# Performance work log

Hardware: AMD Instinct MI355X
Metric: run time of the kernel (lower is better)

Reference implementation:

```python
import jax, jax.numpy as jnp
import numpy as np

HIDDEN = 128
NI = 100000   # ingredient nodes
NT = 100000   # taste nodes
E = 800000    # part_of edges
EPS = 1e-5


def setup_inputs() -> dict:
    key = jax.random.key(0)
    ks = jax.random.split(key, 12)
    s = 1.0 / np.sqrt(HIDDEN)
    return {
        "x_ingredient": jax.random.normal(ks[0], (NI, HIDDEN), jnp.float32),
        "x_taste": jax.random.normal(ks[1], (NT, HIDDEN), jnp.float32),
        "edge_index": jax.random.randint(ks[2], (2, E), 0, 100000, jnp.int64),
        "W_ing": jax.random.normal(ks[3], (HIDDEN, HIDDEN), jnp.float32) * s,
        "b_ing": jax.random.normal(ks[4], (HIDDEN,), jnp.float32) * s,
        "W_taste": jax.random.normal(ks[5], (HIDDEN, HIDDEN), jnp.float32) * s,
        "b_taste": jax.random.normal(ks[6], (HIDDEN,), jnp.float32) * s,
        "att_src": jax.random.normal(ks[7], (HIDDEN,), jnp.float32) * s,
        "att_dst": jax.random.normal(ks[8], (HIDDEN,), jnp.float32) * s,
        "k_lin_W": jax.random.normal(ks[9], (HIDDEN, HIDDEN), jnp.float32) * s,
        "k_lin_b": jax.random.normal(ks[10], (HIDDEN,), jnp.float32) * s,
        "q": jax.random.normal(ks[11], (HIDDEN,), jnp.float32) * s,
        "gamma": jnp.ones((HIDDEN,), jnp.float32),
        "beta": jnp.zeros((HIDDEN,), jnp.float32),
    }


def reference(x_ingredient, x_taste, edge_index, W_ing, b_ing, W_taste, b_taste,
              att_src, att_dst, k_lin_W, k_lin_b, q, gamma, beta):
    # Per-node-type linear projection (HANConv, heads=1)
    h_src = x_ingredient @ W_ing.T + b_ing      # [NI, D]
    h_dst = x_taste @ W_taste.T + b_taste       # [NT, D]

    # Per-node attention logits
    a_src = h_src @ att_src                     # [NI]
    a_dst = h_dst @ att_dst                     # [NT]

    src, dst = edge_index[0], edge_index[1]
    alpha = jax.nn.leaky_relu(a_src[src] + a_dst[dst], negative_slope=0.2)  # [E]

    # Segment softmax over incoming edges of each taste node
    m = jax.ops.segment_max(alpha, dst, num_segments=NT)
    m = jnp.where(jnp.isfinite(m), m, 0.0)      # empty segments -> 0
    e = jnp.exp(alpha - m[dst])
    denom = jax.ops.segment_sum(e, dst, num_segments=NT)
    coef = e / jnp.where(denom[dst] == 0, 1.0, denom[dst])  # [E]

    # Weighted scatter-add aggregation, then per-metapath ReLU (as in HANConv)
    agg = jax.ops.segment_sum(coef[:, None] * h_src[src], dst, num_segments=NT)  # [NT, D]
    agg = jax.nn.relu(agg)

    # Semantic attention across metapaths (single metapath -> weight 1.0)
    w = jnp.tanh(agg @ k_lin_W.T + k_lin_b).mean(0) @ q     # scalar
    beta_sem = jax.nn.softmax(w[None])[0]                   # == 1.0
    out = beta_sem * agg

    # BatchNorm (training statistics) + ReLU
    mu = out.mean(0)
    var = out.var(0)
    out = (out - mu) / jnp.sqrt(var + EPS) * gamma + beta
    return jax.nn.relu(out)
```

## Files before the change

kernel.cpp:

```cpp
#include <hip/hip_runtime.h>
#include <hip/hip_bf16.h>

#define HIDDEN 128
#define NI_N 100000
#define NT_N 100000
#define NE_N 800000
#define EPS_F 1e-5f
#define ELLW 32
#define STATS_B 256
#define ACC_REP 32

#define NB_PROJ 782
#define NB_SC 512
#define SC_THREADS (NB_SC * 256)
#define SC_K 7
#define NB_ADST 3125
#define NB_ZERO 391

typedef __attribute__((ext_vector_type(8))) short bf16x8;
typedef __attribute__((ext_vector_type(4))) float f32x4;

static __device__ __forceinline__ unsigned short f2bf(float f) {
  unsigned u = __float_as_uint(f);
  u += 0x7FFFu + ((u >> 16) & 1u);
  return (unsigned short)(u >> 16);
}

static __device__ __forceinline__ bf16x8 pack8(float4 a, float4 b) {
  bf16x8 r;
  r[0] = (short)f2bf(a.x); r[1] = (short)f2bf(a.y);
  r[2] = (short)f2bf(a.z); r[3] = (short)f2bf(a.w);
  r[4] = (short)f2bf(b.x); r[5] = (short)f2bf(b.y);
  r[6] = (short)f2bf(b.z); r[7] = (short)f2bf(b.w);
  return r;
}

static __device__ __forceinline__ float bf_lo(unsigned int h) {
  return __uint_as_float(h << 16);
}
static __device__ __forceinline__ float bf_hi(unsigned int h) {
  return __uint_as_float(h & 0xffff0000u);
}


__global__ __launch_bounds__(256) void k_pre(const float* __restrict__ W,
                                             const float* __restrict__ b,
                                             const float* __restrict__ att,
                                             float* __restrict__ wbuf,
                                             int* __restrict__ cursor,
                                             float* __restrict__ accum,
                                             int* __restrict__ ticket) {
  int bid = blockIdx.x, t = threadIdx.x;
  if (bid < NB_ZERO) {
    int i = bid * 256 + t;
    if (i < NT_N) cursor[i] = 0;
    return;
  }
  __shared__ float red[128];
#pragma unroll
  for (int r = 0; r < ACC_REP; ++r) accum[r * 256 + t] = 0.f;
  if (t == 0) *ticket = 0;
  if (t < 128) {
    float s = 0.f;
#pragma unroll 8
    for (int c = 0; c < 128; ++c) s += att[c] * W[c * 128 + t];
    wbuf[t] = s;
    red[t] = att[t] * b[t];
  }
  __syncthreads();
  if (t < 64) {
    float v = red[t] + red[t + 64];
    v += __shfl_xor(v, 1);
    v += __shfl_xor(v, 2);
    v += __shfl_xor(v, 4);
    v += __shfl_xor(v, 8);
    v += __shfl_xor(v, 16);
    v += __shfl_xor(v, 32);
    if (t == 0) wbuf[128] = v;
  }
}

__global__ __launch_bounds__(256) void k_main(
    const float* __restrict__ x, const float* __restrict__ W,
    const float* __restrict__ bias, const float* __restrict__ att,
    unsigned int* __restrict__ h32, float* __restrict__ a_src,
    const int* __restrict__ esrc, const int* __restrict__ edst,
    int* __restrict__ cursor, int* __restrict__ ell,
    const float* __restrict__ xt, const float* __restrict__ wbuf,
    float* __restrict__ a_dst) {
  const int t = threadIdx.x;

  if (blockIdx.x >= NB_PROJ && blockIdx.x < NB_PROJ + NB_SC) {
    int base = (blockIdx.x - NB_PROJ) * 256 + t;
    int sv[SC_K], dv[SC_K];
    bool ok[SC_K];
#pragma unroll
    for (int k = 0; k < SC_K; ++k) {
      int e = base + k * SC_THREADS;
      ok[k] = e < NE_N;
      int ec = ok[k] ? e : (NE_N - 1);
      sv[k] = esrc[ec];
      dv[k] = edst[ec];
    }
#pragma unroll
    for (int k = 0; k < SC_K; ++k) {
      if (ok[k]) {
        int pos = atomicAdd(&cursor[dv[k]], 1);
        if (pos < ELLW) ell[dv[k] * ELLW + pos] = sv[k];
      }
    }
    return;
  }

  if (blockIdx.x >= NB_PROJ + NB_SC) {
    __shared__ float swe[128];
    if (t < 128) swe[t] = wbuf[t];
    __syncthreads();
    float be = wbuf[128];
    int lane = t & 63, wv = t >> 6;
    int sub = lane & 7, r = lane >> 3;
    int node = (blockIdx.x - NB_PROJ - NB_SC) * 32 + wv * 8 + r;
    if (node >= NT_N) return;
    const float* xp = xt + (size_t)node * 128 + sub * 4;
    float4 v0 = *(const float4*)(xp);
    float4 v1 = *(const float4*)(xp + 32);
    float4 v2 = *(const float4*)(xp + 64);
    float4 v3 = *(const float4*)(xp + 96);
    const float* wp = swe + sub * 4;
    float4 w0 = *(const float4*)(wp);
    float4 w1 = *(const float4*)(wp + 32);
    float4 w2 = *(const float4*)(wp + 64);
    float4 w3 = *(const float4*)(wp + 96);
    float s = v0.x * w0.x + v0.y * w0.y + v0.z * w0.z + v0.w * w0.w;
    s += v1.x * w1.x + v1.y * w1.y + v1.z * w1.z + v1.w * w1.w;
    s += v2.x * w2.x + v2.y * w2.y + v2.z * w2.z + v2.w * w2.w;
    s += v3.x * w3.x + v3.y * w3.y + v3.z * w3.z + v3.w * w3.w;
    s += __shfl_xor(s, 1);
    s += __shfl_xor(s, 2);
    s += __shfl_xor(s, 4);
    if (sub == 0) a_dst[node] = s + be;
    return;
  }

  const int bid = blockIdx.x;
  __shared__ float sh_a[128];
  if (t < 128) sh_a[t] = 0.f;
  __syncthreads();

  const int wave = t >> 6, lane = t & 63;
  const int colhalf = wave & 1, rowhalf = wave >> 1;
  const int row0 = bid * 128 + rowhalf * 64;
  const int lr = lane & 15;
  const int q = lane >> 4;

  bf16x8 bfrag[4][4];
  float bv[4], av[4];
#pragma unroll
  for (int nt = 0; nt < 4; ++nt) {
    int wrow = colhalf * 64 + nt * 16 + lr;
    const float* wp = W + wrow * 128 + q * 8;
#pragma unroll
    for (int kb = 0; kb < 4; ++kb) {
      float4 wa = *(const float4*)(wp + kb * 32);
      float4 wb = *(const float4*)(wp + kb * 32 + 4);
      bfrag[nt][kb] = pack8(wa, wb);
    }
    bv[nt] = bias[wrow];
    av[nt] = att[wrow];
  }

#pragma unroll
  for (int rt = 0; rt < 4; ++rt) {
    int arow = row0 + rt * 16 + lr;
    int rowc = (arow < NI_N) ? arow : (NI_N - 1);
    const float* xp = x + (size_t)rowc * 128 + q * 8;
    bf16x8 afrag[4];
#pragma unroll
    for (int kb = 0; kb < 4; ++kb) {
      float4 xa = *(const float4*)(xp + kb * 32);
      float4 xb = *(const float4*)(xp + kb * 32 + 4);
      afrag[kb] = pack8(xa, xb);
    }
    float part[4] = {0.f, 0.f, 0.f, 0.f};
    f32x4 cc[4];
#pragma unroll
    for (int nt = 0; nt < 4; ++nt) {
      f32x4 c = {0.f, 0.f, 0.f, 0.f};
#pragma unroll
      for (int kb = 0; kb < 4; ++kb)
        c = __builtin_amdgcn_mfma_f32_16x16x32_bf16(afrag[kb], bfrag[nt][kb], c,
                                                    0, 0, 0);
#pragma unroll
      for (int i = 0; i < 4; ++i) {
        float v = c[i] + bv[nt];
        part[i] += v * av[nt];
        c[i] = v;
      }
      cc[nt] = c;
    }
#pragma unroll
    for (int i = 0; i < 4; ++i) {
      int orow = row0 + rt * 16 + q * 4 + i;
      if (orow < NI_N) {
        unsigned u0 = (unsigned)f2bf(cc[0][i]) | ((unsigned)f2bf(cc[1][i]) << 16);
        unsigned u1 = (unsigned)f2bf(cc[2][i]) | ((unsigned)f2bf(cc[3][i]) << 16);
        unsigned int* hp = h32 + (size_t)orow * 64 + colhalf * 32 + lr;
        hp[0] = u0;
        hp[16] = u1;
      }
      float p = part[i];
      p += __shfl_xor(p, 1);
      p += __shfl_xor(p, 2);
      p += __shfl_xor(p, 4);
      p += __shfl_xor(p, 8);
      if (lr == 0)
        atomicAdd(&sh_a[rowhalf * 64 + rt * 16 + q * 4 + i], p);
    }
  }
  __syncthreads();
  if (t < 128) {
    int row = bid * 128 + t;
    if (row < NI_N) a_src[row] = sh_a[t];
  }
}

__global__ __launch_bounds__(256) void k_agg(const int* __restrict__ deg,
                                             const int* __restrict__ ell,
                                             const float* __restrict__ a_src,
                                             const float* __restrict__ a_dst,
                                             const unsigned int* __restrict__ h32,
                                             unsigned int* __restrict__ aggb) {
  int wv = (blockIdx.x * blockDim.x + threadIdx.x) >> 6;
  int lane = threadIdx.x & 63;
  int half = lane >> 5, l = lane & 31;
  int node = wv * 2 + half;
  if (node >= NT_N) return;
  int n = deg[node];
  n = (n > ELLW) ? ELLW : n;
  float ax = 0.f, ay = 0.f, bx = 0.f, by = 0.f;
  if (n > 0) {
    float ad = a_dst[node];
    int li = (l < n) ? l : (n - 1);
    int sr = ell[node * ELLW + li];
    float al = a_src[sr] + ad;
    al = (al > 0.f) ? al : 0.2f * al;
    float ex = (l < n) ? __expf(al) : 0.f;
    float den = 0.f;
    const int sb = half << 5;
    int n8 = (n + 7) & ~7;
    const uint2* h2 = (const uint2*)h32;
    for (int j = 0; j < n8; j += 8) {
      int s0 = __shfl(sr, sb + j + 0), s1 = __shfl(sr, sb + j + 1);
      int s2 = __shfl(sr, sb + j + 2), s3 = __shfl(sr, sb + j + 3);
      int s4 = __shfl(sr, sb + j + 4), s5 = __shfl(sr, sb + j + 5);
      int s6 = __shfl(sr, sb + j + 6), s7 = __shfl(sr, sb + j + 7);
      float e0 = __shfl(ex, sb + j + 0), e1 = __shfl(ex, sb + j + 1);
      float e2 = __shfl(ex, sb + j + 2), e3 = __shfl(ex, sb + j + 3);
      float e4 = __shfl(ex, sb + j + 4), e5 = __shfl(ex, sb + j + 5);
      float e6 = __shfl(ex, sb + j + 6), e7 = __shfl(ex, sb + j + 7);
      uint2 g0 = h2[s0 * 32 + l];
      uint2 g1 = h2[s1 * 32 + l];
      uint2 g2 = h2[s2 * 32 + l];
      uint2 g3 = h2[s3 * 32 + l];
      uint2 g4 = h2[s4 * 32 + l];
      uint2 g5 = h2[s5 * 32 + l];
      uint2 g6 = h2[s6 * 32 + l];
      uint2 g7 = h2[s7 * 32 + l];
      ax += e0 * bf_lo(g0.x) + e1 * bf_lo(g1.x) + e2 * bf_lo(g2.x) +
            e3 * bf_lo(g3.x) + e4 * bf_lo(g4.x) + e5 * bf_lo(g5.x) +
            e6 * bf_lo(g6.x) + e7 * bf_lo(g7.x);
      ay += e0 * bf_hi(g0.x) + e1 * bf_hi(g1.x) + e2 * bf_hi(g2.x) +
            e3 * bf_hi(g3.x) + e4 * bf_hi(g4.x) + e5 * bf_hi(g5.x) +
            e6 * bf_hi(g6.x) + e7 * bf_hi(g7.x);
      bx += e0 * bf_lo(g0.y) + e1 * bf_lo(g1.y) + e2 * bf_lo(g2.y) +
            e3 * bf_lo(g3.y) + e4 * bf_lo(g4.y) + e5 * bf_lo(g5.y) +
            e6 * bf_lo(g6.y) + e7 * bf_lo(g7.y);
      by += e0 * bf_hi(g0.y) + e1 * bf_hi(g1.y) + e2 * bf_hi(g2.y) +
            e3 * bf_hi(g3.y) + e4 * bf_hi(g4.y) + e5 * bf_hi(g5.y) +
            e6 * bf_hi(g6.y) + e7 * bf_hi(g7.y);
      den += ((e0 + e1) + (e2 + e3)) + ((e4 + e5) + (e6 + e7));
    }
    float inv = 1.f / den;
    ax *= inv; ay *= inv; bx *= inv; by *= inv;
  }
  ax = fmaxf(ax, 0.f);
  ay = fmaxf(ay, 0.f);
  bx = fmaxf(bx, 0.f);
  by = fmaxf(by, 0.f);
  uint2 o;
  o.x = (unsigned)f2bf(ax) | ((unsigned)f2bf(ay) << 16);
  o.y = (unsigned)f2bf(bx) | ((unsigned)f2bf(by) << 16);
  ((uint2*)aggb)[node * 32 + l] = o;
}

__global__ __launch_bounds__(256) void k_stats(const unsigned int* __restrict__ aggb,
                                               float* __restrict__ accum,
                                               const float* __restrict__ gamma,
                                               const float* __restrict__ beta,
                                               float* __restrict__ consts,
                                               int* __restrict__ ticket) {
  __shared__ float red[8][32][8];
  int t = threadIdx.x;
  int p2 = t & 31, g = t >> 5;
  float st[8] = {0.f, 0.f, 0.f, 0.f, 0.f, 0.f, 0.f, 0.f};
  for (int row = blockIdx.x * 8 + g; row < NT_N; row += STATS_B * 8) {
    uint2 v = ((const uint2*)(aggb + (size_t)row * 64))[p2];
    float l0 = bf_lo(v.x), h0 = bf_hi(v.x);
    float l1 = bf_lo(v.y), h1 = bf_hi(v.y);
    st[0] += l0; st[1] += l0 * l0; st[2] += h0; st[3] += h0 * h0;
    st[4] += l1; st[5] += l1 * l1; st[6] += h1; st[7] += h1 * h1;
  }
#pragma unroll
  for (int k = 0; k < 8; ++k) red[g][p2][k] = st[k];
  __syncthreads();
  {
    int p = t >> 2, slot = t & 3;
    int pp2 = p >> 1, u = p & 1;
    float s = 0.f;
#pragma unroll
    for (int gg = 0; gg < 8; ++gg) s += red[gg][pp2][u * 4 + slot];
    atomicAdd(&accum[(blockIdx.x & (ACC_REP - 1)) * 256 + t], s);
  }
  __threadfence();
  __shared__ int amLast;
  if (t == 0) amLast = (atomicAdd(ticket, 1) == STATS_B - 1);
  __syncthreads();
  if (!amLast) return;
  __threadfence();
  __shared__ float fin[256];
  {
    float s = 0.f;
#pragma unroll
    for (int r = 0; r < ACC_REP; ++r) s += accum[r * 256 + t];
    fin[t] = s;
  }
  __syncthreads();
  if (t < 128) {
    int c = t;
    int ch = c >> 6, rem = c & 63;
    int w = rem >> 5, rem2 = rem & 31;
    int half = rem2 >> 4, lr = rem2 & 15;
    int p = ch * 32 + w * 16 + lr;
    float sum = fin[p * 4 + half * 2];
    float sq = fin[p * 4 + half * 2 + 1];
    float mu = sum * (1.f / NT_N);
    float var = sq * (1.f / NT_N) - mu * mu;
    float sc = gamma[c] * rsqrtf(var + EPS_F);
    consts[c] = sc;
    consts[128 + c] = beta[c] - mu * sc;
  }
}

__global__ __launch_bounds__(256) void k_norm(const unsigned int* __restrict__ aggb,
                                              const float* __restrict__ consts,
                                              float* __restrict__ out) {
  __shared__ float sc[256];
  int t = threadIdx.x;
  sc[t] = consts[t];
  __syncthreads();
  int u = blockIdx.x * 256 + t;
  if (u >= NT_N * 16) return;
  uint4 v = ((const uint4*)aggb)[u];
  int wid = u >> 4, k = u & 15;
  int p0 = k * 4;
  int c0 = (p0 >> 5) * 64 + ((p0 >> 4) & 1) * 32 + (p0 & 15);
  unsigned vv[4] = {v.x, v.y, v.z, v.w};
  float o0[4], o1[4];
#pragma unroll
  for (int j = 0; j < 4; ++j) {
    int c = c0 + j;
    float lo = bf_lo(vv[j]), hi = bf_hi(vv[j]);
    o0[j] = fmaxf(lo * sc[c] + sc[128 + c], 0.f);
    o1[j] = fmaxf(hi * sc[c + 16] + sc[144 + c], 0.f);
  }
  float* op = out + (size_t)wid * 128 + c0;
  *(float4*)op = make_float4(o0[0], o0[1], o0[2], o0[3]);
  *(float4*)(op + 16) = make_float4(o1[0], o1[1], o1[2], o1[3]);
}

extern "C" void kernel_launch(void* const* d_in, const int* in_sizes, int n_in,
                              void* d_out, int out_size, void* d_ws, size_t ws_size,
                              hipStream_t stream) {
  const float* x_ing = (const float*)d_in[0];
  const float* x_taste = (const float*)d_in[1];
  const int* edges = (const int*)d_in[2];
  const float* W_ing = (const float*)d_in[3];
  const float* b_ing = (const float*)d_in[4];
  const float* W_taste = (const float*)d_in[5];
  const float* b_taste = (const float*)d_in[6];
  const float* att_src = (const float*)d_in[7];
  const float* att_dst = (const float*)d_in[8];
  const float* gamma = (const float*)d_in[12];
  const float* beta = (const float*)d_in[13];
  float* out = (float*)d_out;
  (void)in_sizes; (void)n_in; (void)out_size; (void)ws_size;

  const int* e_src = edges;
  const int* e_dst = edges + NE_N;

  char* ws = (char*)d_ws;
  size_t off = 0;
  auto alloc = [&](size_t bytes) {
    void* p = ws + off;
    off += (bytes + 255) & ~size_t(255);
    return p;
  };
  unsigned int* h32 = (unsigned int*)alloc(sizeof(unsigned int) * NI_N * 64);
  unsigned int* aggb = (unsigned int*)alloc(sizeof(unsigned int) * NT_N * 64);
  float* a_src = (float*)alloc(sizeof(float) * NI_N);
  float* a_dst = (float*)alloc(sizeof(float) * NT_N);
  float* consts = (float*)alloc(sizeof(float) * 256);
  float* accum = (float*)alloc(sizeof(float) * ACC_REP * 256);
  int* cursor = (int*)alloc(sizeof(int) * NT_N);
  int* ell = (int*)alloc(sizeof(int) * NT_N * ELLW);
  float* wbuf = (float*)alloc(sizeof(float) * 256);
  int* ticket = (int*)alloc(sizeof(int) * 64);

  k_pre<<<NB_ZERO + 1, 256, 0, stream>>>(W_taste, b_taste, att_dst, wbuf,
                                         cursor, accum, ticket);
  k_main<<<NB_PROJ + NB_SC + NB_ADST, 256, 0, stream>>>(
      x_ing, W_ing, b_ing, att_src, h32, a_src, e_src, e_dst, cursor, ell,
      x_taste, wbuf, a_dst);
  k_agg<<<((NT_N + 1) / 2 * 64 + 255) / 256, 256, 0, stream>>>(
      cursor, ell, a_src, a_dst, h32, aggb);
  k_stats<<<STATS_B, 256, 0, stream>>>(aggb, accum, gamma, beta, consts,
                                       ticket);
  k_norm<<<(NT_N * 16 + 255) / 256, 256, 0, stream>>>(aggb, consts, out);
}
```

Before: 294.1 us.

## Interleave projection, edge scatter, and a_dst blocks across the fused grid

```diff
diff --git a/kernel.cpp b/kernel.cpp
--- a/kernel.cpp
+++ b/kernel.cpp
@@ -11,10 +11,11 @@
 #define ACC_REP 32
 
 #define NB_PROJ 782
-#define NB_SC 512
+#define NB_SC 520
 #define SC_THREADS (NB_SC * 256)
 #define SC_K 7
 #define NB_ADST 3125
+#define NB_MAIN (NB_PROJ + NB_SC + NB_ADST)
 #define NB_ZERO 391
 
 typedef __attribute__((ext_vector_type(8))) short bf16x8;
@@ -90,8 +91,20 @@
     float* __restrict__ a_dst) {
   const int t = threadIdx.x;
 
-  if (blockIdx.x >= NB_PROJ && blockIdx.x < NB_PROJ + NB_SC) {
-    int base = (blockIdx.x - NB_PROJ) * 256 + t;
+  const int i = blockIdx.x;
+  const int m5 = i % 5, d5 = i / 5;
+  int role, rid;
+  if (m5 == 0 && d5 < NB_PROJ) {
+    role = 0; rid = d5;
+  } else {
+    int projBefore = (i < NB_PROJ * 5) ? (d5 + (m5 ? 1 : 0)) : NB_PROJ;
+    int r = i - projBefore;
+    if (r % 7 == 6) { role = 1; rid = r / 7; }
+    else            { role = 2; rid = r - (r + 1) / 7; }
+  }
+
+  if (role == 1) {
+    int base = rid * 256 + t;
     int sv[SC_K], dv[SC_K];
     bool ok[SC_K];
 #pragma unroll
@@ -112,14 +125,14 @@
     return;
   }
 
-  if (blockIdx.x >= NB_PROJ + NB_SC) {
+  if (role == 2) {
     __shared__ float swe[128];
     if (t < 128) swe[t] = wbuf[t];
     __syncthreads();
     float be = wbuf[128];
     int lane = t & 63, wv = t >> 6;
     int sub = lane & 7, r = lane >> 3;
-    int node = (blockIdx.x - NB_PROJ - NB_SC) * 32 + wv * 8 + r;
+    int node = rid * 32 + wv * 8 + r;
     if (node >= NT_N) return;
     const float* xp = xt + (size_t)node * 128 + sub * 4;
     float4 v0 = *(const float4*)(xp);
@@ -142,7 +155,7 @@
     return;
   }
 
-  const int bid = blockIdx.x;
+  const int bid = rid;
   __shared__ float sh_a[128];
   if (t < 128) sh_a[t] = 0.f;
   __syncthreads();
@@ -191,30 +204,30 @@
         c = __builtin_amdgcn_mfma_f32_16x16x32_bf16(afrag[kb], bfrag[nt][kb], c,
                                                     0, 0, 0);
 #pragma unroll
-      for (int i = 0; i < 4; ++i) {
-        float v = c[i] + bv[nt];
-        part[i] += v * av[nt];
-        c[i] = v;
+      for (int ii = 0; ii < 4; ++ii) {
+        float v = c[ii] + bv[nt];
+        part[ii] += v * av[nt];
+        c[ii] = v;
       }
       cc[nt] = c;
     }
 #pragma unroll
-    for (int i = 0; i < 4; ++i) {
-      int orow = row0 + rt * 16 + q * 4 + i;
+    for (int ii = 0; ii < 4; ++ii) {
+      int orow = row0 + rt * 16 + q * 4 + ii;
       if (orow < NI_N) {
-        unsigned u0 = (unsigned)f2bf(cc[0][i]) | ((unsigned)f2bf(cc[1][i]) << 16);
-        unsigned u1 = (unsigned)f2bf(cc[2][i]) | ((unsigned)f2bf(cc[3][i]) << 16);
+        unsigned u0 = (unsigned)f2bf(cc[0][ii]) | ((unsigned)f2bf(cc[1][ii]) << 16);
+        unsigned u1 = (unsigned)f2bf(cc[2][ii]) | ((unsigned)f2bf(cc[3][ii]) << 16);
         unsigned int* hp = h32 + (size_t)orow * 64 + colhalf * 32 + lr;
         hp[0] = u0;
         hp[16] = u1;
       }
-      float p = part[i];
+      float p = part[ii];
       p += __shfl_xor(p, 1);
       p += __shfl_xor(p, 2);
       p += __shfl_xor(p, 4);
       p += __shfl_xor(p, 8);
       if (lr == 0)
-        atomicAdd(&sh_a[rowhalf * 64 + rt * 16 + q * 4 + i], p);
+        atomicAdd(&sh_a[rowhalf * 64 + rt * 16 + q * 4 + ii], p);
     }
   }
   __syncthreads();
@@ -418,7 +431,7 @@
 
   k_pre<<<NB_ZERO + 1, 256, 0, stream>>>(W_taste, b_taste, att_dst, wbuf,
                                          cursor, accum, ticket);
-  k_main<<<NB_PROJ + NB_SC + NB_ADST, 256, 0, stream>>>(
+  k_main<<<NB_MAIN, 256, 0, stream>>>(
       x_ing, W_ing, b_ing, att_src, h32, a_src, e_src, e_dst, cursor, ell,
       x_taste, wbuf, a_dst);
   k_agg<<<((NT_N + 1) / 2 * 64 + 255) / 256, 256, 0, stream>>>(
```

After: 297.0 us. No clear change (+1.0%).

## Fuse aggregation, BN stats and normalize into one cooperative persistent kernel

Applied to the files above, without the earlier changes.

```diff
diff --git a/kernel.cpp b/kernel.cpp
--- a/kernel.cpp
+++ b/kernel.cpp
@@ -1,5 +1,8 @@
 #include <hip/hip_runtime.h>
+#include <hip/hip_cooperative_groups.h>
 #include <hip/hip_bf16.h>
+
+namespace cg = cooperative_groups;
 
 #define HIDDEN 128
 #define NI_N 100000
@@ -7,7 +10,6 @@
 #define NE_N 800000
 #define EPS_F 1e-5f
 #define ELLW 32
-#define STATS_B 256
 #define ACC_REP 32
 
 #define NB_PROJ 782
@@ -16,6 +18,7 @@
 #define SC_K 7
 #define NB_ADST 3125
 #define NB_ZERO 391
+#define NW_AGG ((NT_N + 1) / 2)
 
 typedef __attribute__((ext_vector_type(8))) short bf16x8;
 typedef __attribute__((ext_vector_type(4))) float f32x4;
@@ -48,8 +51,7 @@
                                              const float* __restrict__ att,
                                              float* __restrict__ wbuf,
                                              int* __restrict__ cursor,
-                                             float* __restrict__ accum,
-                                             int* __restrict__ ticket) {
+                                             float* __restrict__ accum) {
   int bid = blockIdx.x, t = threadIdx.x;
   if (bid < NB_ZERO) {
     int i = bid * 256 + t;
@@ -59,7 +61,6 @@
   __shared__ float red[128];
 #pragma unroll
   for (int r = 0; r < ACC_REP; ++r) accum[r * 256 + t] = 0.f;
-  if (t == 0) *ticket = 0;
   if (t < 128) {
     float s = 0.f;
 #pragma unroll 8
@@ -224,158 +225,141 @@
   }
 }
 
-__global__ __launch_bounds__(256) void k_agg(const int* __restrict__ deg,
-                                             const int* __restrict__ ell,
-                                             const float* __restrict__ a_src,
-                                             const float* __restrict__ a_dst,
-                                             const unsigned int* __restrict__ h32,
-                                             unsigned int* __restrict__ aggb) {
-  int wv = (blockIdx.x * blockDim.x + threadIdx.x) >> 6;
-  int lane = threadIdx.x & 63;
-  int half = lane >> 5, l = lane & 31;
-  int node = wv * 2 + half;
-  if (node >= NT_N) return;
-  int n = deg[node];
-  n = (n > ELLW) ? ELLW : n;
-  float ax = 0.f, ay = 0.f, bx = 0.f, by = 0.f;
-  if (n > 0) {
-    float ad = a_dst[node];
-    int li = (l < n) ? l : (n - 1);
-    int sr = ell[node * ELLW + li];
-    float al = a_src[sr] + ad;
-    al = (al > 0.f) ? al : 0.2f * al;
-    float ex = (l < n) ? __expf(al) : 0.f;
-    float den = 0.f;
-    const int sb = half << 5;
-    int n8 = (n + 7) & ~7;
-    const uint2* h2 = (const uint2*)h32;
-    for (int j = 0; j < n8; j += 8) {
-      int s0 = __shfl(sr, sb + j + 0), s1 = __shfl(sr, sb + j + 1);
-      int s2 = __shfl(sr, sb + j + 2), s3 = __shfl(sr, sb + j + 3);
-      int s4 = __shfl(sr, sb + j + 4), s5 = __shfl(sr, sb + j + 5);
-      int s6 = __shfl(sr, sb + j + 6), s7 = __shfl(sr, sb + j + 7);
-      float e0 = __shfl(ex, sb + j + 0), e1 = __shfl(ex, sb + j + 1);
-      float e2 = __shfl(ex, sb + j + 2), e3 = __shfl(ex, sb + j + 3);
-      float e4 = __shfl(ex, sb + j + 4), e5 = __shfl(ex, sb + j + 5);
-      float e6 = __shfl(ex, sb + j + 6), e7 = __shfl(ex, sb + j + 7);
-      uint2 g0 = h2[s0 * 32 + l];
-      uint2 g1 = h2[s1 * 32 + l];
-      uint2 g2 = h2[s2 * 32 + l];
-      uint2 g3 = h2[s3 * 32 + l];
-      uint2 g4 = h2[s4 * 32 + l];
-      uint2 g5 = h2[s5 * 32 + l];
-      uint2 g6 = h2[s6 * 32 + l];
-      uint2 g7 = h2[s7 * 32 + l];
-      ax += e0 * bf_lo(g0.x) + e1 * bf_lo(g1.x) + e2 * bf_lo(g2.x) +
-            e3 * bf_lo(g3.x) + e4 * bf_lo(g4.x) + e5 * bf_lo(g5.x) +
-            e6 * bf_lo(g6.x) + e7 * bf_lo(g7.x);
-      ay += e0 * bf_hi(g0.x) + e1 * bf_hi(g1.x) + e2 * bf_hi(g2.x) +
-            e3 * bf_hi(g3.x) + e4 * bf_hi(g4.x) + e5 * bf_hi(g5.x) +
-            e6 * bf_hi(g6.x) + e7 * bf_hi(g7.x);
-      bx += e0 * bf_lo(g0.y) + e1 * bf_lo(g1.y) + e2 * bf_lo(g2.y) +
-            e3 * bf_lo(g3.y) + e4 * bf_lo(g4.y) + e5 * bf_lo(g5.y) +
-            e6 * bf_lo(g6.y) + e7 * bf_lo(g7.y);
-      by += e0 * bf_hi(g0.y) + e1 * bf_hi(g1.y) + e2 * bf_hi(g2.y) +
-            e3 * bf_hi(g3.y) + e4 * bf_hi(g4.y) + e5 * bf_hi(g5.y) +
-            e6 * bf_hi(g6.y) + e7 * bf_hi(g7.y);
-      den += ((e0 + e1) + (e2 + e3)) + ((e4 + e5) + (e6 + e7));
-    }
-    float inv = 1.f / den;
-    ax *= inv; ay *= inv; bx *= inv; by *= inv;
-  }
-  ax = fmaxf(ax, 0.f);
-  ay = fmaxf(ay, 0.f);
-  bx = fmaxf(bx, 0.f);
-  by = fmaxf(by, 0.f);
-  uint2 o;
-  o.x = (unsigned)f2bf(ax) | ((unsigned)f2bf(ay) << 16);
-  o.y = (unsigned)f2bf(bx) | ((unsigned)f2bf(by) << 16);
-  ((uint2*)aggb)[node * 32 + l] = o;
-}
-
-__global__ __launch_bounds__(256) void k_stats(const unsigned int* __restrict__ aggb,
-                                               float* __restrict__ accum,
-                                               const float* __restrict__ gamma,
-                                               const float* __restrict__ beta,
-                                               float* __restrict__ consts,
-                                               int* __restrict__ ticket) {
-  __shared__ float red[8][32][8];
-  int t = threadIdx.x;
-  int p2 = t & 31, g = t >> 5;
+__global__ __launch_bounds__(256) void k_aggnorm(
+    const int* __restrict__ deg, const int* __restrict__ ell,
+    const float* __restrict__ a_src, const float* __restrict__ a_dst,
+    const unsigned int* __restrict__ h32, unsigned int* __restrict__ aggb,
+    float* __restrict__ accum, const float* __restrict__ gamma,
+    const float* __restrict__ beta, float* __restrict__ out) {
+  const int t = threadIdx.x;
+  const int bid = blockIdx.x;
+  const int G = gridDim.x;
+  cg::grid_group grid = cg::this_grid();
+
+  __shared__ float red[8][32][9];
+  __shared__ float sc[256];
+
+  const int wave = t >> 6, lane = t & 63;
+  const int half = lane >> 5, l = lane & 31;
+  const int sb = half << 5;
+  const uint2* h2 = (const uint2*)h32;
+
   float st[8] = {0.f, 0.f, 0.f, 0.f, 0.f, 0.f, 0.f, 0.f};
-  for (int row = blockIdx.x * 8 + g; row < NT_N; row += STATS_B * 8) {
-    uint2 v = ((const uint2*)(aggb + (size_t)row * 64))[p2];
-    float l0 = bf_lo(v.x), h0 = bf_hi(v.x);
-    float l1 = bf_lo(v.y), h1 = bf_hi(v.y);
-    st[0] += l0; st[1] += l0 * l0; st[2] += h0; st[3] += h0 * h0;
-    st[4] += l1; st[5] += l1 * l1; st[6] += h1; st[7] += h1 * h1;
-  }
-#pragma unroll
-  for (int k = 0; k < 8; ++k) red[g][p2][k] = st[k];
-  __syncthreads();
+  for (int wv = bid * 4 + wave; wv < NW_AGG; wv += G * 4) {
+    int node = wv * 2 + half;
+    int n = deg[node];
+    n = (n > ELLW) ? ELLW : n;
+    float ax = 0.f, ay = 0.f, bx = 0.f, by = 0.f;
+    if (n > 0) {
+      float ad = a_dst[node];
+      int li = (l < n) ? l : (n - 1);
+      int sr = ell[node * ELLW + li];
+      float al = a_src[sr] + ad;
+      al = (al > 0.f) ? al : 0.2f * al;
+      float ex = (l < n) ? __expf(al) : 0.f;
+      float den = 0.f;
+      int n8 = (n + 7) & ~7;
+      for (int j = 0; j < n8; j += 8) {
+        int s0 = __shfl(sr, sb + j + 0), s1 = __shfl(sr, sb + j + 1);
+        int s2 = __shfl(sr, sb + j + 2), s3 = __shfl(sr, sb + j + 3);
+        int s4 = __shfl(sr, sb + j + 4), s5 = __shfl(sr, sb + j + 5);
+        int s6 = __shfl(sr, sb + j + 6), s7 = __shfl(sr, sb + j + 7);
+        float e0 = __shfl(ex, sb + j + 0), e1 = __shfl(ex, sb + j + 1);
+        float e2 = __shfl(ex, sb + j + 2), e3 = __shfl(ex, sb + j + 3);
+        float e4 = __shfl(ex, sb + j + 4), e5 = __shfl(ex, sb + j + 5);
+        float e6 = __shfl(ex, sb + j + 6), e7 = __shfl(ex, sb + j + 7);
+        uint2 g0 = h2[s0 * 32 + l];
+        uint2 g1 = h2[s1 * 32 + l];
+        uint2 g2 = h2[s2 * 32 + l];
+        uint2 g3 = h2[s3 * 32 + l];
+        uint2 g4 = h2[s4 * 32 + l];
+        uint2 g5 = h2[s5 * 32 + l];
+        uint2 g6 = h2[s6 * 32 + l];
+        uint2 g7 = h2[s7 * 32 + l];
+        ax += e0 * bf_lo(g0.x) + e1 * bf_lo(g1.x) + e2 * bf_lo(g2.x) +
+              e3 * bf_lo(g3.x) + e4 * bf_lo(g4.x) + e5 * bf_lo(g5.x) +
+              e6 * bf_lo(g6.x) + e7 * bf_lo(g7.x);
+        ay += e0 * bf_hi(g0.x) + e1 * bf_hi(g1.x) + e2 * bf_hi(g2.x) +
+              e3 * bf_hi(g3.x) + e4 * bf_hi(g4.x) + e5 * bf_hi(g5.x) +
+              e6 * bf_hi(g6.x) + e7 * bf_hi(g7.x);
+        bx += e0 * bf_lo(g0.y) + e1 * bf_lo(g1.y) + e2 * bf_lo(g2.y) +
+              e3 * bf_lo(g3.y) + e4 * bf_lo(g4.y) + e5 * bf_lo(g5.y) +
+              e6 * bf_lo(g6.y) + e7 * bf_lo(g7.y);
+        by += e0 * bf_hi(g0.y) + e1 * bf_hi(g1.y) + e2 * bf_hi(g2.y) +
+              e3 * bf_hi(g3.y) + e4 * bf_hi(g4.y) + e5 * bf_hi(g5.y) +
+              e6 * bf_hi(g6.y) + e7 * bf_hi(g7.y);
+        den += ((e0 + e1) + (e2 + e3)) + ((e4 + e5) + (e6 + e7));
+      }
+      float inv = 1.f / den;
+      ax *= inv; ay *= inv; bx *= inv; by *= inv;
+    }
+    ax = fmaxf(ax, 0.f);
+    ay = fmaxf(ay, 0.f);
+    bx = fmaxf(bx, 0.f);
+    by = fmaxf(by, 0.f);
+    uint2 o;
+    o.x = (unsigned)f2bf(ax) | ((unsigned)f2bf(ay) << 16);
+    o.y = (unsigned)f2bf(bx) | ((unsigned)f2bf(by) << 16);
+    ((uint2*)aggb)[node * 32 + l] = o;
+    st[0] += ax; st[1] += ax * ax; st[2] += ay; st[3] += ay * ay;
+    st[4] += bx; st[5] += bx * bx; st[6] += by; st[7] += by * by;
+  }
   {
+    int hw = wave * 2 + half;
+#pragma unroll
+    for (int k = 0; k < 8; ++k) red[hw][l][k] = st[k];
+    __syncthreads();
     int p = t >> 2, slot = t & 3;
     int pp2 = p >> 1, u = p & 1;
     float s = 0.f;
 #pragma unroll
     for (int gg = 0; gg < 8; ++gg) s += red[gg][pp2][u * 4 + slot];
-    atomicAdd(&accum[(blockIdx.x & (ACC_REP - 1)) * 256 + t], s);
-  }
-  __threadfence();
-  __shared__ int amLast;
-  if (t == 0) amLast = (atomicAdd(ticket, 1) == STATS_B - 1);
-  __syncthreads();
-  if (!amLast) return;
-  __threadfence();
-  __shared__ float fin[256];
+    atomicAdd(&accum[(bid & (ACC_REP - 1)) * 256 + t], s);
+  }
+  grid.sync();
+
   {
     float s = 0.f;
 #pragma unroll
     for (int r = 0; r < ACC_REP; ++r) s += accum[r * 256 + t];
-    fin[t] = s;
-  }
-  __syncthreads();
-  if (t < 128) {
-    int c = t;
-    int ch = c >> 6, rem = c & 63;
-    int w = rem >> 5, rem2 = rem & 31;
-    int half = rem2 >> 4, lr = rem2 & 15;
-    int p = ch * 32 + w * 16 + lr;
-    float sum = fin[p * 4 + half * 2];
-    float sq = fin[p * 4 + half * 2 + 1];
-    float mu = sum * (1.f / NT_N);
-    float var = sq * (1.f / NT_N) - mu * mu;
-    float sc = gamma[c] * rsqrtf(var + EPS_F);
-    consts[c] = sc;
-    consts[128 + c] = beta[c] - mu * sc;
-  }
-}
-
-__global__ __launch_bounds__(256) void k_norm(const unsigned int* __restrict__ aggb,
-                                              const float* __restrict__ consts,
-                                              float* __restrict__ out) {
-  __shared__ float sc[256];
-  int t = threadIdx.x;
-  sc[t] = consts[t];
-  __syncthreads();
-  int u = blockIdx.x * 256 + t;
-  if (u >= NT_N * 16) return;
-  uint4 v = ((const uint4*)aggb)[u];
-  int wid = u >> 4, k = u & 15;
-  int p0 = k * 4;
-  int c0 = (p0 >> 5) * 64 + ((p0 >> 4) & 1) * 32 + (p0 & 15);
-  unsigned vv[4] = {v.x, v.y, v.z, v.w};
-  float o0[4], o1[4];
-#pragma unroll
-  for (int j = 0; j < 4; ++j) {
-    int c = c0 + j;
-    float lo = bf_lo(vv[j]), hi = bf_hi(vv[j]);
-    o0[j] = fmaxf(lo * sc[c] + sc[128 + c], 0.f);
-    o1[j] = fmaxf(hi * sc[c + 16] + sc[144 + c], 0.f);
-  }
-  float* op = out + (size_t)wid * 128 + c0;
-  *(float4*)op = make_float4(o0[0], o0[1], o0[2], o0[3]);
-  *(float4*)(op + 16) = make_float4(o1[0], o1[1], o1[2], o1[3]);
+    float* redf = &red[0][0][0];
+    redf[t] = s;
+    __syncthreads();
+    if (t < 128) {
+      int c = t;
+      int ch = c >> 6, rem = c & 63;
+      int w = rem >> 5, rem2 = rem & 31;
+      int hf = rem2 >> 4, lr = rem2 & 15;
+      int p = ch * 32 + w * 16 + lr;
+      float sum = redf[p * 4 + hf * 2];
+      float sq = redf[p * 4 + hf * 2 + 1];
+      float mu = sum * (1.f / NT_N);
+      float var = sq * (1.f / NT_N) - mu * mu;
+      float scv = gamma[c] * rsqrtf(var + EPS_F);
+      sc[c] = scv;
+      sc[128 + c] = beta[c] - mu * scv;
+    }
+    __syncthreads();
+  }
+
+  for (int u = bid * 256 + t; u < NT_N * 16; u += G * 256) {
+    uint4 v = ((const uint4*)aggb)[u];
+    int wid = u >> 4, k = u & 15;
+    int p0 = k * 4;
+    int c0 = (p0 >> 5) * 64 + ((p0 >> 4) & 1) * 32 + (p0 & 15);
+    unsigned vv[4] = {v.x, v.y, v.z, v.w};
+    float o0[4], o1[4];
+#pragma unroll
+    for (int j = 0; j < 4; ++j) {
+      int c = c0 + j;
+      float lo = bf_lo(vv[j]), hi = bf_hi(vv[j]);
+      o0[j] = fmaxf(lo * sc[c] + sc[128 + c], 0.f);
+      o1[j] = fmaxf(hi * sc[c + 16] + sc[144 + c], 0.f);
+    }
+    float* op = out + (size_t)wid * 128 + c0;
+    *(float4*)op = make_float4(o0[0], o0[1], o0[2], o0[3]);
+    *(float4*)(op + 16) = make_float4(o1[0], o1[1], o1[2], o1[3]);
+  }
 }
 
 extern "C" void kernel_launch(void* const* d_in, const int* in_sizes, int n_in,
@@ -409,21 +393,36 @@
   unsigned int* aggb = (unsigned int*)alloc(sizeof(unsigned int) * NT_N * 64);
   float* a_src = (float*)alloc(sizeof(float) * NI_N);
   float* a_dst = (float*)alloc(sizeof(float) * NT_N);
-  float* consts = (float*)alloc(sizeof(float) * 256);
   float* accum = (float*)alloc(sizeof(float) * ACC_REP * 256);
   int* cursor = (int*)alloc(sizeof(int) * NT_N);
   int* ell = (int*)alloc(sizeof(int) * NT_N * ELLW);
   float* wbuf = (float*)alloc(sizeof(float) * 256);
-  int* ticket = (int*)alloc(sizeof(int) * 64);
+
+  static int g_grid = 0;
+  if (g_grid == 0) {
+    int dev = 0;
+    (void)hipGetDevice(&dev);
+    int cu = 256;
+    (void)hipDeviceGetAttribute(&cu, hipDeviceAttributeMultiprocessorCount,
+                                dev);
+    int nb = 0;
+    if (hipOccupancyMaxActiveBlocksPerMultiprocessor(&nb, k_aggnorm, 256, 0) !=
+            hipSuccess ||
+        nb < 1)
+      nb = 1;
+    long g = (long)nb * cu;
+    if (g > 2048) g = 2048;
+    g_grid = (int)g;
+  }
 
   k_pre<<<NB_ZERO + 1, 256, 0, stream>>>(W_taste, b_taste, att_dst, wbuf,
-                                         cursor, accum, ticket);
+                                         cursor, accum);
   k_main<<<NB_PROJ + NB_SC + NB_ADST, 256, 0, stream>>>(
       x_ing, W_ing, b_ing, att_src, h32, a_src, e_src, e_dst, cursor, ell,
       x_taste, wbuf, a_dst);
-  k_agg<<<((NT_N + 1) / 2 * 64 + 255) / 256, 256, 0, stream>>>(
-      cursor, ell, a_src, a_dst, h32, aggb);
-  k_stats<<<STATS_B, 256, 0, stream>>>(aggb, accum, gamma, beta, consts,
-                                       ticket);
-  k_norm<<<(NT_N * 16 + 255) / 256, 256, 0, stream>>>(aggb, consts, out);
-}
+  void* args[] = {(void*)&cursor, (void*)&ell,   (void*)&a_src,
+                  (void*)&a_dst,  (void*)&h32,   (void*)&aggb,
+                  (void*)&accum,  (void*)&gamma, (void*)&beta, (void*)&out};
+  hipLaunchCooperativeKernel(k_aggnorm, dim3(g_grid), dim3(256), args, 0,
+                             stream);
+}
```

Result: slower. 374.4 us (+27.3%).

## Fuse BatchNorm statistics accumulation into aggregation kernel, add tiny consts kernel

Applied to the files above, without the earlier changes.

```diff
diff --git a/kernel.cpp b/kernel.cpp
--- a/kernel.cpp
+++ b/kernel.cpp
@@ -7,8 +7,7 @@
 #define NE_N 800000
 #define EPS_F 1e-5f
 #define ELLW 32
-#define STATS_B 256
-#define ACC_REP 32
+#define ACC_REP 128
 
 #define NB_PROJ 782
 #define NB_SC 512
@@ -48,8 +47,7 @@
                                              const float* __restrict__ att,
                                              float* __restrict__ wbuf,
                                              int* __restrict__ cursor,
-                                             float* __restrict__ accum,
-                                             int* __restrict__ ticket) {
+                                             float* __restrict__ accum) {
   int bid = blockIdx.x, t = threadIdx.x;
   if (bid < NB_ZERO) {
     int i = bid * 256 + t;
@@ -57,9 +55,8 @@
     return;
   }
   __shared__ float red[128];
-#pragma unroll
+#pragma unroll 8
   for (int r = 0; r < ACC_REP; ++r) accum[r * 256 + t] = 0.f;
-  if (t == 0) *ticket = 0;
   if (t < 128) {
     float s = 0.f;
 #pragma unroll 8
@@ -229,12 +226,13 @@
                                              const float* __restrict__ a_src,
                                              const float* __restrict__ a_dst,
                                              const unsigned int* __restrict__ h32,
-                                             unsigned int* __restrict__ aggb) {
-  int wv = (blockIdx.x * blockDim.x + threadIdx.x) >> 6;
-  int lane = threadIdx.x & 63;
+                                             unsigned int* __restrict__ aggb,
+                                             float* __restrict__ accum) {
+  const int t = threadIdx.x;
+  int wv = (blockIdx.x * blockDim.x + t) >> 6;
+  int lane = t & 63;
   int half = lane >> 5, l = lane & 31;
   int node = wv * 2 + half;
-  if (node >= NT_N) return;
   int n = deg[node];
   n = (n > ELLW) ? ELLW : n;
   float ax = 0.f, ay = 0.f, bx = 0.f, by = 0.f;
@@ -291,27 +289,13 @@
   o.x = (unsigned)f2bf(ax) | ((unsigned)f2bf(ay) << 16);
   o.y = (unsigned)f2bf(bx) | ((unsigned)f2bf(by) << 16);
   ((uint2*)aggb)[node * 32 + l] = o;
-}
-
-__global__ __launch_bounds__(256) void k_stats(const unsigned int* __restrict__ aggb,
-                                               float* __restrict__ accum,
-                                               const float* __restrict__ gamma,
-                                               const float* __restrict__ beta,
-                                               float* __restrict__ consts,
-                                               int* __restrict__ ticket) {
+
   __shared__ float red[8][32][8];
-  int t = threadIdx.x;
-  int p2 = t & 31, g = t >> 5;
-  float st[8] = {0.f, 0.f, 0.f, 0.f, 0.f, 0.f, 0.f, 0.f};
-  for (int row = blockIdx.x * 8 + g; row < NT_N; row += STATS_B * 8) {
-    uint2 v = ((const uint2*)(aggb + (size_t)row * 64))[p2];
-    float l0 = bf_lo(v.x), h0 = bf_hi(v.x);
-    float l1 = bf_lo(v.y), h1 = bf_hi(v.y);
-    st[0] += l0; st[1] += l0 * l0; st[2] += h0; st[3] += h0 * h0;
-    st[4] += l1; st[5] += l1 * l1; st[6] += h1; st[7] += h1 * h1;
-  }
-#pragma unroll
-  for (int k = 0; k < 8; ++k) red[g][p2][k] = st[k];
+  int hw = (t >> 6) * 2 + half;
+  red[hw][l][0] = ax; red[hw][l][1] = ax * ax;
+  red[hw][l][2] = ay; red[hw][l][3] = ay * ay;
+  red[hw][l][4] = bx; red[hw][l][5] = bx * bx;
+  red[hw][l][6] = by; red[hw][l][7] = by * by;
   __syncthreads();
   {
     int p = t >> 2, slot = t & 3;
@@ -321,19 +305,18 @@
     for (int gg = 0; gg < 8; ++gg) s += red[gg][pp2][u * 4 + slot];
     atomicAdd(&accum[(blockIdx.x & (ACC_REP - 1)) * 256 + t], s);
   }
-  __threadfence();
-  __shared__ int amLast;
-  if (t == 0) amLast = (atomicAdd(ticket, 1) == STATS_B - 1);
-  __syncthreads();
-  if (!amLast) return;
-  __threadfence();
+}
+
+__global__ __launch_bounds__(256) void k_consts(const float* __restrict__ accum,
+                                                const float* __restrict__ gamma,
+                                                const float* __restrict__ beta,
+                                                float* __restrict__ consts) {
   __shared__ float fin[256];
-  {
-    float s = 0.f;
-#pragma unroll
-    for (int r = 0; r < ACC_REP; ++r) s += accum[r * 256 + t];
-    fin[t] = s;
-  }
+  int t = threadIdx.x;
+  float s = 0.f;
+#pragma unroll 8
+  for (int r = 0; r < ACC_REP; ++r) s += accum[r * 256 + t];
+  fin[t] = s;
   __syncthreads();
   if (t < 128) {
     int c = t;
@@ -410,20 +393,18 @@
   float* a_src = (float*)alloc(sizeof(float) * NI_N);
   float* a_dst = (float*)alloc(sizeof(float) * NT_N);
   float* consts = (float*)alloc(sizeof(float) * 256);
+  float* wbuf = (float*)alloc(sizeof(float) * 256);
   float* accum = (float*)alloc(sizeof(float) * ACC_REP * 256);
   int* cursor = (int*)alloc(sizeof(int) * NT_N);
   int* ell = (int*)alloc(sizeof(int) * NT_N * ELLW);
-  float* wbuf = (float*)alloc(sizeof(float) * 256);
-  int* ticket = (int*)alloc(sizeof(int) * 64);
 
   k_pre<<<NB_ZERO + 1, 256, 0, stream>>>(W_taste, b_taste, att_dst, wbuf,
-                                         cursor, accum, ticket);
+                                         cursor, accum);
   k_main<<<NB_PROJ + NB_SC + NB_ADST, 256, 0, stream>>>(
       x_ing, W_ing, b_ing, att_src, h32, a_src, e_src, e_dst, cursor, ell,
       x_taste, wbuf, a_dst);
   k_agg<<<((NT_N + 1) / 2 * 64 + 255) / 256, 256, 0, stream>>>(
-      cursor, ell, a_src, a_dst, h32, aggb);
-  k_stats<<<STATS_B, 256, 0, stream>>>(aggb, accum, gamma, beta, consts,
-                                       ticket);
+      cursor, ell, a_src, a_dst, h32, aggb, accum);
+  k_consts<<<1, 256, 0, stream>>>(accum, gamma, beta, consts);
   k_norm<<<(NT_N * 16 + 255) / 256, 256, 0, stream>>>(aggb, consts, out);
 }
```

Result: faster. 275.6 us, median of 2 (-6.3%).
